# Kernel optimization log

Hardware: AMD Instinct MI355X
Metric: run time of the kernel (lower is better)

## Reference

```python
import jax, jax.numpy as jnp
import numpy as np

KS = 3          # spline kernel size per dim (kernel_size[0] repeated over dim)
DIM = 3
S = 2 ** DIM    # basis terms for degree-1 B-spline
K = KS ** DIM   # total kernel weight slots
CIN, COUT = 8, 16
N, V, T = 2, 1024, 32
E0 = 8192


def spline_basis(pseudo):
    # pseudo: [E, DIM] in [0,1]; degree-1 open B-splines, kernel size KS per dim
    v = pseudo * (KS - 1)                                   # open spline: u*(K-1)
    fl = jnp.floor(v)
    frac = v - fl
    fl = fl.astype(jnp.int32)
    bits = (jnp.arange(S, dtype=jnp.int32)[:, None] >> jnp.arange(DIM, dtype=jnp.int32)[None, :]) & 1  # [S, DIM]
    idx = (fl[:, None, :] + bits[None, :, :]) % KS          # [E, S, DIM]
    strides = (KS ** jnp.arange(DIM, dtype=jnp.int32))      # stride for dim d = KS^d
    wi = jnp.sum(idx * strides[None, None, :], axis=-1)     # [E, S] weight indices
    fac = jnp.where(bits[None, :, :] == 0, 1.0 - frac[:, None, :], frac[:, None, :])
    basis = jnp.prod(fac, axis=-1)                          # [E, S]
    return basis, wi


def setup_inputs() -> dict:
    key = jax.random.key(0)
    ks = jax.random.split(key, 8)
    x = jax.random.normal(ks[0], (N, V, CIN, T), dtype=jnp.float32)
    edge_index = jax.random.randint(ks[1], (2, N * E0), 0, V, dtype=jnp.int32)
    edge_attr = jax.random.uniform(ks[2], (N * E0, DIM), dtype=jnp.float32)
    bound = 1.0 / np.sqrt(CIN * K)
    weight = jax.random.uniform(ks[3], (K, CIN, COUT), jnp.float32, -bound, bound)
    root = jax.random.uniform(ks[4], (CIN, COUT), jnp.float32, -bound, bound)
    bias = jax.random.uniform(ks[5], (COUT,), jnp.float32, -bound, bound)
    cb = 1.0 / np.sqrt(CIN)
    conv_w = jax.random.uniform(ks[6], (COUT, CIN), jnp.float32, -cb, cb)
    conv_b = jax.random.uniform(ks[7], (COUT,), jnp.float32, -cb, cb)
    return {"x": x, "edge_index": edge_index, "edge_attr": edge_attr,
            "weight": weight, "root": root, "bias": bias,
            "conv_w": conv_w, "conv_b": conv_b}


def reference(x, edge_index, edge_attr, weight, root, bias, conv_w, conv_b):
    n_batch, n_nodes, c_in, t_len = x.shape
    c_out = root.shape[1]
    # residual branch: 1x1 Conv2d over [N, C, T, V] + ELU
    xp = jnp.transpose(x, (0, 2, 3, 1))                     # [N, C, T, V]
    res = jax.nn.elu(jnp.einsum('nctv,oc->notv', xp, conv_w) + conv_b[None, :, None, None])
    # flatten nodes: [T, N, V, C] -> [T*N*V, C]
    xf = jnp.transpose(x, (3, 0, 1, 2)).reshape(-1, c_in)
    n_total = xf.shape[0]
    # expand(): keep first E0 edges, replicate over N*T graph copies with node offset
    e0 = edge_index.shape[1] // n_batch
    ei = edge_index[:, :e0]
    ea = edge_attr[:e0]
    offsets = jnp.arange(n_batch * t_len, dtype=ei.dtype) * n_nodes
    edges = (ei[:, None, :] + offsets[None, :, None]).reshape(2, -1)   # [2, E]
    attrs = jnp.tile(ea, (n_batch * t_len, 1))                          # [E, DIM]
    row, col = edges[0], edges[1]
    basis, wi = spline_basis(attrs)                          # [E,S], [E,S]
    x_col = xf[col]                                          # [E, C] gather
    out_e = jnp.zeros((row.shape[0], c_out), x.dtype)
    for s in range(S):                                       # S=8 fixed small loop
        Wg = weight[wi[:, s]]                                # [E, C, Cout] gather
        out_e = out_e + basis[:, s, None] * jnp.einsum('ei,eio->eo', x_col, Wg)
    agg = jax.ops.segment_sum(out_e, row, num_segments=n_total)  # scatter-add (norm=False)
    g = jax.nn.elu(agg + xf @ root + bias)
    g = g.reshape(t_len, n_batch, n_nodes, c_out).transpose(1, 3, 0, 2)  # [N, Cout, T, V]
    out = jax.nn.elu(g + res)
    return jnp.transpose(out, (0, 3, 1, 2))                  # [N, V, Cout, T]
```

## Files before the change

kernel.cpp:

```cpp
#include <hip/hip_runtime.h>
#include <math.h>

#define NV 1024
#define NCIN 8
#define NCOUT 16
#define NT 32
#define NBATCH 2
#define NE0 8192
#define EIDX_STRIDE 16384

__device__ __forceinline__ float elu_f(float x) {
    return x > 0.0f ? x : (expf(x) - 1.0f);
}

__global__ void compute_we(const float* __restrict__ ea,
                           const float* __restrict__ weight,
                           float* __restrict__ We) {
    int tid = blockIdx.x * blockDim.x + threadIdx.x;
    int e = tid >> 7;
    int j = tid & 127;
    if (e >= NE0) return;
    float p0 = ea[e * 3 + 0] * 2.0f;
    float p1 = ea[e * 3 + 1] * 2.0f;
    float p2 = ea[e * 3 + 2] * 2.0f;
    float f0 = floorf(p0), f1 = floorf(p1), f2 = floorf(p2);
    float r0 = p0 - f0, r1 = p1 - f1, r2 = p2 - f2;
    int i0 = (int)f0, i1 = (int)f1, i2 = (int)f2;
    float acc = 0.0f;
#pragma unroll
    for (int s = 0; s < 8; ++s) {
        int b0 = s & 1, b1 = (s >> 1) & 1, b2 = (s >> 2) & 1;
        int wi = (i0 + b0) + 3 * (i1 + b1) + 9 * (i2 + b2);
        float bas = (b0 ? r0 : 1.0f - r0) *
                    (b1 ? r1 : 1.0f - r1) *
                    (b2 ? r2 : 1.0f - r2);
        acc += bas * weight[wi * 128 + j];
    }
    We[e * 128 + j] = acc;
}

__global__ void hist_kernel(const int* __restrict__ eidx, int* __restrict__ counts) {
    int e = blockIdx.x * blockDim.x + threadIdx.x;
    if (e < NE0) atomicAdd(&counts[eidx[e]], 1);
}

__global__ void scan_kernel(const int* __restrict__ counts,
                            int* __restrict__ starts,
                            int* __restrict__ cursor) {
    __shared__ int tmp[NV];
    int tid = threadIdx.x;
    tmp[tid] = counts[tid];
    __syncthreads();
#pragma unroll
    for (int off = 1; off < NV; off <<= 1) {
        int v = (tid >= off) ? tmp[tid - off] : 0;
        __syncthreads();
        tmp[tid] += v;
        __syncthreads();
    }
    if (tid == 0) starts[0] = 0;
    starts[tid + 1] = tmp[tid];
    cursor[tid] = (tid == 0) ? 0 : tmp[tid - 1];
}

__global__ void scatter_kernel(const int* __restrict__ eidx,
                               int* __restrict__ cursor,
                               int* __restrict__ elist) {
    int e = blockIdx.x * blockDim.x + threadIdx.x;
    if (e >= NE0) return;
    int d = eidx[e];
    int src = eidx[EIDX_STRIDE + e];
    int pos = atomicAdd(&cursor[d], 1);
    elist[pos] = (e << 10) | src;
}

__global__ __launch_bounds__(256) void spatial_main(
    const float* __restrict__ x,
    const float* __restrict__ We,
    const int* __restrict__ starts,
    const int* __restrict__ elist,
    const float* __restrict__ root,
    const float* __restrict__ bias,
    const float* __restrict__ conv_w,
    const float* __restrict__ conv_b,
    float* __restrict__ out)
{
    int wave = threadIdx.x >> 6;
    int lane = threadIdx.x & 63;
    int d = blockIdx.x * 4 + wave;
    int n = lane & 1;
    int t = lane >> 1;

    const float* xn = x + (size_t)n * NV * NCIN * NT;

    float xs[NCIN];
#pragma unroll
    for (int c = 0; c < NCIN; ++c)
        xs[c] = xn[((size_t)d * NCIN + c) * NT + t];

    float acc[NCOUT];
#pragma unroll
    for (int o = 0; o < NCOUT; ++o) acc[o] = 0.0f;

    int s0 = starts[d];
    int s1 = starts[d + 1];
    for (int i = s0; i < s1; ++i) {
        int packed = __builtin_amdgcn_readfirstlane(elist[i]);
        int e = packed >> 10;
        int src = packed & 1023;
        float xc[NCIN];
#pragma unroll
        for (int c = 0; c < NCIN; ++c)
            xc[c] = xn[((size_t)src * NCIN + c) * NT + t];
        const float* W = We + (size_t)e * 128;
#pragma unroll
        for (int c = 0; c < NCIN; ++c) {
#pragma unroll
            for (int o = 0; o < NCOUT; ++o)
                acc[o] += xc[c] * W[c * 16 + o];
        }
    }

#pragma unroll
    for (int o = 0; o < NCOUT; ++o) {
        float r = bias[o];
#pragma unroll
        for (int c = 0; c < NCIN; ++c) r += xs[c] * root[c * NCOUT + o];
        float cv = conv_b[o];
#pragma unroll
        for (int c = 0; c < NCIN; ++c) cv += xs[c] * conv_w[o * NCIN + c];
        float res = elu_f(cv);
        float gv = elu_f(acc[o] + r);
        float ov = elu_f(gv + res);
        out[(((size_t)n * NV + d) * NCOUT + o) * NT + t] = ov;
    }
}

extern "C" void kernel_launch(void* const* d_in, const int* in_sizes, int n_in,
                              void* d_out, int out_size, void* d_ws, size_t ws_size,
                              hipStream_t stream) {
    const float* x      = (const float*)d_in[0];
    const int*   eidx   = (const int*)d_in[1];
    const float* ea     = (const float*)d_in[2];
    const float* weight = (const float*)d_in[3];
    const float* root   = (const float*)d_in[4];
    const float* bias   = (const float*)d_in[5];
    const float* conv_w = (const float*)d_in[6];
    const float* conv_b = (const float*)d_in[7];
    float* out = (float*)d_out;

    char* ws = (char*)d_ws;
    float* We    = (float*)(ws);
    int*   counts = (int*)(ws + 4194304);
    int*   starts = (int*)(ws + 4198400);
    int*   cursor = (int*)(ws + 4202752);
    int*   elist  = (int*)(ws + 4206848);

    hipMemsetAsync(counts, 0, NV * sizeof(int), stream);
    compute_we<<<dim3((NE0 * 128) / 256), dim3(256), 0, stream>>>(ea, weight, We);
    hist_kernel<<<dim3(NE0 / 256), dim3(256), 0, stream>>>(eidx, counts);
    scan_kernel<<<dim3(1), dim3(NV), 0, stream>>>(counts, starts, cursor);
    scatter_kernel<<<dim3(NE0 / 256), dim3(256), 0, stream>>>(eidx, cursor, elist);
    spatial_main<<<dim3(NV / 4), dim3(256), 0, stream>>>(x, We, starts, elist,
                                                         root, bias, conv_w, conv_b, out);
}
```

Baseline: 103.9 us.

## Fuse prep kernels into one launch and split node edges across four waves

Merges the We computation, histogram, scan and CSR scatter into a single prep kernel, with one extra block doing the CSR build in shared memory. This removes the memset and three launches along with their serialization. spatial_main now gives each destination node a full block of four waves that stride over its edges, then reduces partial sums through shared memory, which raises parallelism per node. The trade-off is that the CSR build runs serially in one block, and the main kernel pays for an added shared-memory reduction and a barrier.

```diff
diff --git a/kernel.cpp b/kernel.cpp
--- a/kernel.cpp
+++ b/kernel.cpp
@@ -5,89 +5,94 @@
 #define NCIN 8
 #define NCOUT 16
 #define NT 32
-#define NBATCH 2
 #define NE0 8192
 #define EIDX_STRIDE 16384
+#define WE_BLOCKS 4096
 
 __device__ __forceinline__ float elu_f(float x) {
     return x > 0.0f ? x : (expf(x) - 1.0f);
 }
 
-__global__ void compute_we(const float* __restrict__ ea,
-                           const float* __restrict__ weight,
-                           float* __restrict__ We) {
-    int tid = blockIdx.x * blockDim.x + threadIdx.x;
-    int e = tid >> 7;
-    int j = tid & 127;
-    if (e >= NE0) return;
-    float p0 = ea[e * 3 + 0] * 2.0f;
-    float p1 = ea[e * 3 + 1] * 2.0f;
-    float p2 = ea[e * 3 + 2] * 2.0f;
-    float f0 = floorf(p0), f1 = floorf(p1), f2 = floorf(p2);
-    float r0 = p0 - f0, r1 = p1 - f1, r2 = p2 - f2;
-    int i0 = (int)f0, i1 = (int)f1, i2 = (int)f2;
-    float acc = 0.0f;
+__global__ __launch_bounds__(256) void prep_kernel(
+    const float* __restrict__ ea,
+    const int*   __restrict__ eidx,
+    const float* __restrict__ weight,
+    float* __restrict__ We,
+    int*   __restrict__ starts_g,
+    int*   __restrict__ elist)
+{
+    if (blockIdx.x < WE_BLOCKS) {
+        int tid = blockIdx.x * 256 + threadIdx.x;
+        int e = tid >> 7;
+        int j = tid & 127;
+        float p0 = ea[e * 3 + 0] * 2.0f;
+        float p1 = ea[e * 3 + 1] * 2.0f;
+        float p2 = ea[e * 3 + 2] * 2.0f;
+        float f0 = floorf(p0), f1 = floorf(p1), f2 = floorf(p2);
+        float r0 = p0 - f0, r1 = p1 - f1, r2 = p2 - f2;
+        int i0 = (int)f0, i1 = (int)f1, i2 = (int)f2;
+        float acc = 0.0f;
 #pragma unroll
-    for (int s = 0; s < 8; ++s) {
-        int b0 = s & 1, b1 = (s >> 1) & 1, b2 = (s >> 2) & 1;
-        int wi = (i0 + b0) + 3 * (i1 + b1) + 9 * (i2 + b2);
-        float bas = (b0 ? r0 : 1.0f - r0) *
-                    (b1 ? r1 : 1.0f - r1) *
-                    (b2 ? r2 : 1.0f - r2);
-        acc += bas * weight[wi * 128 + j];
+        for (int s = 0; s < 8; ++s) {
+            int b0 = s & 1, b1 = (s >> 1) & 1, b2 = (s >> 2) & 1;
+            int wi = (i0 + b0) + 3 * (i1 + b1) + 9 * (i2 + b2);
+            float bas = (b0 ? r0 : 1.0f - r0) *
+                        (b1 ? r1 : 1.0f - r1) *
+                        (b2 ? r2 : 1.0f - r2);
+            acc += bas * weight[wi * 128 + j];
+        }
+        We[e * 128 + j] = acc;
+        return;
     }
-    We[e * 128 + j] = acc;
-}
 
-__global__ void hist_kernel(const int* __restrict__ eidx, int* __restrict__ counts) {
-    int e = blockIdx.x * blockDim.x + threadIdx.x;
-    if (e < NE0) atomicAdd(&counts[eidx[e]], 1);
-}
-
-__global__ void scan_kernel(const int* __restrict__ counts,
-                            int* __restrict__ starts,
-                            int* __restrict__ cursor) {
-    __shared__ int tmp[NV];
-    int tid = threadIdx.x;
-    tmp[tid] = counts[tid];
+    __shared__ int cnt[NV];
+    __shared__ int cur[NV];
+    __shared__ int tsum[256];
+    int t = threadIdx.x;
+    for (int i = t; i < NV; i += 256) cnt[i] = 0;
+    __syncthreads();
+    for (int e = t; e < NE0; e += 256) atomicAdd(&cnt[eidx[e]], 1);
+    __syncthreads();
+    int c0 = cnt[4 * t], c1 = cnt[4 * t + 1], c2 = cnt[4 * t + 2], c3 = cnt[4 * t + 3];
+    int s = c0 + c1 + c2 + c3;
+    tsum[t] = s;
     __syncthreads();
 #pragma unroll
-    for (int off = 1; off < NV; off <<= 1) {
-        int v = (tid >= off) ? tmp[tid - off] : 0;
+    for (int off = 1; off < 256; off <<= 1) {
+        int v = (t >= off) ? tsum[t - off] : 0;
         __syncthreads();
-        tmp[tid] += v;
+        tsum[t] += v;
         __syncthreads();
     }
-    if (tid == 0) starts[0] = 0;
-    starts[tid + 1] = tmp[tid];
-    cursor[tid] = (tid == 0) ? 0 : tmp[tid - 1];
-}
-
-__global__ void scatter_kernel(const int* __restrict__ eidx,
-                               int* __restrict__ cursor,
-                               int* __restrict__ elist) {
-    int e = blockIdx.x * blockDim.x + threadIdx.x;
-    if (e >= NE0) return;
-    int d = eidx[e];
-    int src = eidx[EIDX_STRIDE + e];
-    int pos = atomicAdd(&cursor[d], 1);
-    elist[pos] = (e << 10) | src;
+    int base = tsum[t] - s;
+    starts_g[4 * t] = base;     cur[4 * t] = base;     base += c0;
+    starts_g[4 * t + 1] = base; cur[4 * t + 1] = base; base += c1;
+    starts_g[4 * t + 2] = base; cur[4 * t + 2] = base; base += c2;
+    starts_g[4 * t + 3] = base; cur[4 * t + 3] = base;
+    if (t == 255) starts_g[NV] = NE0;
+    __syncthreads();
+    for (int e = t; e < NE0; e += 256) {
+        int d = eidx[e];
+        int src = eidx[EIDX_STRIDE + e];
+        int pos = atomicAdd(&cur[d], 1);
+        elist[pos] = (e << 10) | src;
+    }
 }
 
 __global__ __launch_bounds__(256) void spatial_main(
     const float* __restrict__ x,
     const float* __restrict__ We,
-    const int* __restrict__ starts,
-    const int* __restrict__ elist,
+    const int*   __restrict__ starts,
+    const int*   __restrict__ elist,
     const float* __restrict__ root,
     const float* __restrict__ bias,
     const float* __restrict__ conv_w,
     const float* __restrict__ conv_b,
     float* __restrict__ out)
 {
-    int wave = threadIdx.x >> 6;
+    int w = threadIdx.x >> 6;
     int lane = threadIdx.x & 63;
-    int d = blockIdx.x * 4 + wave;
+    int d = blockIdx.x;
     int n = lane & 1;
     int t = lane >> 1;
 
@@ -104,7 +109,7 @@
 
     int s0 = starts[d];
     int s1 = starts[d + 1];
-    for (int i = s0; i < s1; ++i) {
+    for (int i = s0 + w; i < s1; i += 4) {
         int packed = __builtin_amdgcn_readfirstlane(elist[i]);
         int e = packed >> 10;
         int src = packed & 1023;
@@ -121,8 +126,15 @@
         }
     }
 
+    __shared__ float red[4][64][17];
 #pragma unroll
-    for (int o = 0; o < NCOUT; ++o) {
+    for (int o = 0; o < NCOUT; ++o) red[w][lane][o] = acc[o];
+    __syncthreads();
+
+#pragma unroll
+    for (int oo = 0; oo < 4; ++oo) {
+        int o = 4 * w + oo;
+        float a = red[0][lane][o] + red[1][lane][o] + red[2][lane][o] + red[3][lane][o];
         float r = bias[o];
 #pragma unroll
         for (int c = 0; c < NCIN; ++c) r += xs[c] * root[c * NCOUT + o];
@@ -130,9 +142,8 @@
 #pragma unroll
         for (int c = 0; c < NCIN; ++c) cv += xs[c] * conv_w[o * NCIN + c];
         float res = elu_f(cv);
-        float gv = elu_f(acc[o] + r);
-        float ov = elu_f(gv + res);
-        out[(((size_t)n * NV + d) * NCOUT + o) * NT + t] = ov;
+        float gv = elu_f(a + r);
+        out[(((size_t)n * NV + d) * NCOUT + o) * NT + t] = elu_f(gv + res);
     }
 }
 
@@ -150,17 +161,12 @@
     float* out = (float*)d_out;
 
     char* ws = (char*)d_ws;
-    float* We    = (float*)(ws);
-    int*   counts = (int*)(ws + 4194304);
-    int*   starts = (int*)(ws + 4198400);
-    int*   cursor = (int*)(ws + 4202752);
-    int*   elist  = (int*)(ws + 4206848);
+    float* We     = (float*)(ws);
+    int*   starts = (int*)(ws + 4194304);
+    int*   elist  = (int*)(ws + 4198404);
 
-    hipMemsetAsync(counts, 0, NV * sizeof(int), stream);
-    compute_we<<<dim3((NE0 * 128) / 256), dim3(256), 0, stream>>>(ea, weight, We);
-    hist_kernel<<<dim3(NE0 / 256), dim3(256), 0, stream>>>(eidx, counts);
-    scan_kernel<<<dim3(1), dim3(NV), 0, stream>>>(counts, starts, cursor);
-    scatter_kernel<<<dim3(NE0 / 256), dim3(256), 0, stream>>>(eidx, cursor, elist);
-    spatial_main<<<dim3(NV / 4), dim3(256), 0, stream>>>(x, We, starts, elist,
-                                                         root, bias, conv_w, conv_b, out);
+    prep_kernel<<<dim3(WE_BLOCKS + 1), dim3(256), 0, stream>>>(ea, eidx, weight,
+                                                               We, starts, elist);
+    spatial_main<<<dim3(NV), dim3(256), 0, stream>>>(x, We, starts, elist,
+                                                     root, bias, conv_w, conv_b, out);
 }
```

After: 99.72 us. 1.04x faster.
